# Kernel optimization log

Measured on AMD Instinct MI355X. Metric: run time of the kernel, lower is better.

## Reference

```python
import jax, jax.numpy as jnp
import numpy as np

N_NODES = 35
N_EDGES = 1190
N_VIEWS = 6
C1_IN, C1_OUT = 1, 256
C2_IN, C2_OUT = 256, 256
C3_IN, C3_OUT = 256, 64


def _nnconv(x, edge_attr, src, dst, nn_w, nn_b, lin_w, bias, c_in, c_out):
    """PyG NNConv with aggr='mean': per-edge MLP weight, gather-matvec-scatter."""
    # per-edge weight matrices: [E, c_in, c_out]
    W = jax.nn.relu(edge_attr @ nn_w.T + nn_b).reshape(-1, c_in, c_out)
    # gather source features and apply per-edge weight: [E, c_out]
    msg = jnp.einsum('ei,eio->eo', x[src], W)
    # scatter-mean into target nodes
    agg = jax.ops.segment_sum(msg, dst, num_segments=N_NODES)
    cnt = jax.ops.segment_sum(jnp.ones((msg.shape[0],), msg.dtype), dst,
                              num_segments=N_NODES)
    agg = agg / jnp.maximum(cnt, 1.0)[:, None]
    # root transform (lin has no bias in PyG) + conv bias
    return agg + x @ lin_w.T + bias


def setup_inputs() -> dict:
    key = jax.random.key(0)
    ks = jax.random.split(key, 16)
    s = 0.05
    x = jnp.ones((N_NODES, C1_IN), jnp.float32)
    edge_attr = jax.random.uniform(ks[0], (N_EDGES, N_VIEWS), jnp.float32)
    edge_index = jax.random.randint(ks[1], (2, N_EDGES), 0, N_NODES, jnp.int32)
    inp = {
        'x': x, 'edge_attr': edge_attr, 'edge_index': edge_index,
        'nn1_w': jax.random.normal(ks[2], (C1_IN * C1_OUT, N_VIEWS), jnp.float32) * s,
        'nn1_b': jax.random.normal(ks[3], (C1_IN * C1_OUT,), jnp.float32) * s,
        'lin1_w': jax.random.normal(ks[4], (C1_OUT, C1_IN), jnp.float32) * s,
        'b1': jax.random.normal(ks[5], (C1_OUT,), jnp.float32) * s,
        'nn2_w': jax.random.normal(ks[6], (C2_IN * C2_OUT, N_VIEWS), jnp.float32) * s,
        'nn2_b': jax.random.normal(ks[7], (C2_IN * C2_OUT,), jnp.float32) * s,
        'lin2_w': jax.random.normal(ks[8], (C2_OUT, C2_IN), jnp.float32) * s,
        'b2': jax.random.normal(ks[9], (C2_OUT,), jnp.float32) * s,
        'nn3_w': jax.random.normal(ks[10], (C3_IN * C3_OUT, N_VIEWS), jnp.float32) * s,
        'nn3_b': jax.random.normal(ks[11], (C3_IN * C3_OUT,), jnp.float32) * s,
        'lin3_w': jax.random.normal(ks[12], (C3_OUT, C3_IN), jnp.float32) * s,
        'b3': jax.random.normal(ks[13], (C3_OUT,), jnp.float32) * s,
    }
    return inp


def reference(x, edge_attr, edge_index, nn1_w, nn1_b, lin1_w, b1,
              nn2_w, nn2_b, lin2_w, b2, nn3_w, nn3_b, lin3_w, b3):
    src, dst = edge_index[0], edge_index[1]
    x = jax.nn.relu(_nnconv(x, edge_attr, src, dst, nn1_w, nn1_b, lin1_w, b1, C1_IN, C1_OUT))
    x = jax.nn.relu(_nnconv(x, edge_attr, src, dst, nn2_w, nn2_b, lin2_w, b2, C2_IN, C2_OUT))
    x = jax.nn.relu(_nnconv(x, edge_attr, src, dst, nn3_w, nn3_b, lin3_w, b3, C3_IN, C3_OUT))
    # CBT: pairwise L1 distances over feature dim -> [N, N]
    # (equivalent to repeat(35,1,1) / transpose / abs / sum since N == 35)
    cbt = jnp.abs(x[None, :, :] - x[:, None, :]).sum(-1)
    return cbt
```

## Files before the change

### kernel.cpp

```cpp
#include <hip/hip_runtime.h>


#define NN 35
#define NE 1190
#define TE 10
#define NG 119

__global__ void zero_k(float* p, int n) {
    int t = blockIdx.x * 256 + threadIdx.x;
    if (t < n) p[t] = 0.f;
}

__global__ __launch_bounds__(512) void msg1_k(
    const float* __restrict__ x, const float* __restrict__ ea,
    const int* __restrict__ ei, const float* __restrict__ w1,
    const float* __restrict__ b1w, float* __restrict__ agg1,
    float* __restrict__ cnt) {
    int tid = threadIdx.x;
    int e = blockIdx.x * 2 + (tid >> 8);
    int o = tid & 255;
    int src = ei[e];
    int dst = ei[NE + e];
    float xs = x[src];
    const float* eap = ea + e * 6;
    const float* w = w1 + o * 6;
    float d = b1w[o];
#pragma unroll
    for (int v = 0; v < 6; v++) d = fmaf(eap[v], w[v], d);
    atomicAdd(agg1 + dst * 256 + o, xs * fmaxf(d, 0.f));
    if (o == 0) atomicAdd(cnt + dst, 1.0f);
}

__global__ __launch_bounds__(256) void x1_k(
    const float* __restrict__ x, const float* __restrict__ lin1,
    const float* __restrict__ b1, const float* __restrict__ agg1,
    const float* __restrict__ cnt, float* __restrict__ x1) {
    int n = blockIdx.x, o = threadIdx.x;
    float c = fmaxf(cnt[n], 1.f);
    float v = agg1[n * 256 + o] / c + x[n] * lin1[o] + b1[o];
    x1[n * 256 + o] = fmaxf(v, 0.f);
}

__global__ __launch_bounds__(512, 4) void msg2_k(
    const float* __restrict__ x1, const float* __restrict__ ea,
    const int* __restrict__ ei, const float* __restrict__ w2,
    const float* __restrict__ b2w, float* __restrict__ agg2) {
    __shared__ __attribute__((aligned(16))) float xs[TE][256];
    __shared__ float eas[TE][6];
    __shared__ int dsts[TE];
    __shared__ int srcs[TE];
    __shared__ float part[7][TE][64];
    int tid = threadIdx.x;
    int eg = blockIdx.x >> 2;
    int og = blockIdx.x & 3;
    int e0 = eg * TE;
    if (tid < TE) { dsts[tid] = ei[NE + e0 + tid]; srcs[tid] = ei[e0 + tid]; }
    if (tid >= 64 && tid < 64 + TE * 6) {
        int t = tid - 64;
        eas[t / 6][t % 6] = ea[e0 * 6 + t];
    }
    __syncthreads();
    for (int idx = tid; idx < TE * 64; idx += 512) {
        int te = idx >> 6, q = idx & 63;
        ((float4*)xs[te])[q] = ((const float4*)(x1 + srcs[te] * 256))[q];
    }
    __syncthreads();
    int ol = tid & 63;
    int o = og * 64 + ol;
    int ic = tid >> 6;
    float eareg[TE][6];
#pragma unroll
    for (int te = 0; te < TE; te++)
#pragma unroll
        for (int v = 0; v < 6; v++) eareg[te][v] = eas[te][v];
    float acc[TE] = {};
    for (int ii = 0; ii < 32; ii++) {
        int i = ic * 32 + ii;
        const float* w = w2 + (size_t)(i * 256 + o) * 6;
        float2 wa = *(const float2*)w;
        float2 wb = *(const float2*)(w + 2);
        float2 wc = *(const float2*)(w + 4);
        float b = b2w[i * 256 + o];
#pragma unroll
        for (int te = 0; te < TE; te += 2) {
            float dx = b, dy = b;
            dx = fmaf(eareg[te][0], wa.x, dx); dy = fmaf(eareg[te + 1][0], wa.x, dy);
            dx = fmaf(eareg[te][1], wa.y, dx); dy = fmaf(eareg[te + 1][1], wa.y, dy);
            dx = fmaf(eareg[te][2], wb.x, dx); dy = fmaf(eareg[te + 1][2], wb.x, dy);
            dx = fmaf(eareg[te][3], wb.y, dx); dy = fmaf(eareg[te + 1][3], wb.y, dy);
            dx = fmaf(eareg[te][4], wc.x, dx); dy = fmaf(eareg[te + 1][4], wc.x, dy);
            dx = fmaf(eareg[te][5], wc.y, dx); dy = fmaf(eareg[te + 1][5], wc.y, dy);
            dx = fmaxf(dx, 0.f);               dy = fmaxf(dy, 0.f);
            acc[te] = fmaf(xs[te][i], dx, acc[te]);
            acc[te + 1] = fmaf(xs[te + 1][i], dy, acc[te + 1]);
        }
    }
    if (ic > 0) {
#pragma unroll
        for (int te = 0; te < TE; te++) part[ic - 1][te][ol] = acc[te];
    }
    __syncthreads();
    if (ic == 0) {
#pragma unroll
        for (int te = 0; te < TE; te++) {
            float s = acc[te];
#pragma unroll
            for (int p = 0; p < 7; p++) s += part[p][te][ol];
            atomicAdd(agg2 + dsts[te] * 256 + o, s);
        }
    }
}

__global__ __launch_bounds__(1024) void x2_k(
    const float* __restrict__ x1, const float* __restrict__ lin2,
    const float* __restrict__ b2, const float* __restrict__ agg2,
    const float* __restrict__ cnt, float* __restrict__ x2) {
    __shared__ float xr[256];
    __shared__ float part[3][256];
    int n = blockIdx.x, tid = threadIdx.x;
    int o = tid & 255, ic = tid >> 8;
    if (tid < 256) xr[tid] = x1[n * 256 + tid];
    __syncthreads();
    const float4* w = (const float4*)(lin2 + (size_t)o * 256 + ic * 64);
    float s = 0.f;
#pragma unroll
    for (int k = 0; k < 16; k++) {
        float4 wv = w[k];
        int i = ic * 64 + k * 4;
        s = fmaf(wv.x, xr[i], s);
        s = fmaf(wv.y, xr[i + 1], s);
        s = fmaf(wv.z, xr[i + 2], s);
        s = fmaf(wv.w, xr[i + 3], s);
    }
    if (ic > 0) part[ic - 1][o] = s;
    __syncthreads();
    if (ic == 0) {
        float tot = s + part[0][o] + part[1][o] + part[2][o];
        float c = fmaxf(cnt[n], 1.f);
        float v = agg2[n * 256 + o] / c + tot + b2[o];
        x2[n * 256 + o] = fmaxf(v, 0.f);
    }
}

__global__ __launch_bounds__(512, 4) void msg3_k(
    const float* __restrict__ x2, const float* __restrict__ ea,
    const int* __restrict__ ei, const float* __restrict__ w3,
    const float* __restrict__ b3w, float* __restrict__ agg3) {
    __shared__ __attribute__((aligned(16))) float xs[TE][64];
    __shared__ float eas[TE][6];
    __shared__ int dsts[TE];
    __shared__ int srcs[TE];
    __shared__ float part[7][TE][64];
    int tid = threadIdx.x;
    int eg = blockIdx.x >> 2;
    int ig = blockIdx.x & 3;
    int e0 = eg * TE;
    if (tid < TE) { dsts[tid] = ei[NE + e0 + tid]; srcs[tid] = ei[e0 + tid]; }
    if (tid >= 64 && tid < 64 + TE * 6) {
        int t = tid - 64;
        eas[t / 6][t % 6] = ea[e0 * 6 + t];
    }
    __syncthreads();
    for (int idx = tid; idx < TE * 16; idx += 512) {
        int te = idx >> 4, q = idx & 15;
        ((float4*)xs[te])[q] =
            ((const float4*)(x2 + srcs[te] * 256 + ig * 64))[q];
    }
    __syncthreads();
    int ol = tid & 63;
    int ic = tid >> 6;
    float eareg[TE][6];
#pragma unroll
    for (int te = 0; te < TE; te++)
#pragma unroll
        for (int v = 0; v < 6; v++) eareg[te][v] = eas[te][v];
    float acc[TE] = {};
    for (int jj = 0; jj < 8; jj++) {
        int ii = ic * 8 + jj;
        int i = ig * 64 + ii;
        const float* w = w3 + (size_t)(i * 64 + ol) * 6;
        float2 wa = *(const float2*)w;
        float2 wb = *(const float2*)(w + 2);
        float2 wc = *(const float2*)(w + 4);
        float b = b3w[i * 64 + ol];
#pragma unroll
        for (int te = 0; te < TE; te += 2) {
            float dx = b, dy = b;
            dx = fmaf(eareg[te][0], wa.x, dx); dy = fmaf(eareg[te + 1][0], wa.x, dy);
            dx = fmaf(eareg[te][1], wa.y, dx); dy = fmaf(eareg[te + 1][1], wa.y, dy);
            dx = fmaf(eareg[te][2], wb.x, dx); dy = fmaf(eareg[te + 1][2], wb.x, dy);
            dx = fmaf(eareg[te][3], wb.y, dx); dy = fmaf(eareg[te + 1][3], wb.y, dy);
            dx = fmaf(eareg[te][4], wc.x, dx); dy = fmaf(eareg[te + 1][4], wc.x, dy);
            dx = fmaf(eareg[te][5], wc.y, dx); dy = fmaf(eareg[te + 1][5], wc.y, dy);
            dx = fmaxf(dx, 0.f);               dy = fmaxf(dy, 0.f);
            acc[te] = fmaf(xs[te][ii], dx, acc[te]);
            acc[te + 1] = fmaf(xs[te + 1][ii], dy, acc[te + 1]);
        }
    }
    if (ic > 0) {
#pragma unroll
        for (int te = 0; te < TE; te++) part[ic - 1][te][ol] = acc[te];
    }
    __syncthreads();
    if (ic == 0) {
#pragma unroll
        for (int te = 0; te < TE; te++) {
            float s = acc[te];
#pragma unroll
            for (int p = 0; p < 7; p++) s += part[p][te][ol];
            atomicAdd(agg3 + dsts[te] * 64 + ol, s);
        }
    }
}

__global__ __launch_bounds__(256) void x3_k(
    const float* __restrict__ x2, const float* __restrict__ lin3,
    const float* __restrict__ b3, const float* __restrict__ agg3,
    const float* __restrict__ cnt, float* __restrict__ x3) {
    __shared__ float xr[256];
    __shared__ float part[3][64];
    int n = blockIdx.x, tid = threadIdx.x;
    int o = tid & 63, ic = tid >> 6;
    xr[tid] = x2[n * 256 + tid];
    __syncthreads();
    const float4* w = (const float4*)(lin3 + (size_t)o * 256 + ic * 64);
    float s = 0.f;
#pragma unroll
    for (int k = 0; k < 16; k++) {
        float4 wv = w[k];
        int i = ic * 64 + k * 4;
        s = fmaf(wv.x, xr[i], s);
        s = fmaf(wv.y, xr[i + 1], s);
        s = fmaf(wv.z, xr[i + 2], s);
        s = fmaf(wv.w, xr[i + 3], s);
    }
    if (ic > 0) part[ic - 1][o] = s;
    __syncthreads();
    if (ic == 0) {
        float tot = s + part[0][o] + part[1][o] + part[2][o];
        float c = fmaxf(cnt[n], 1.f);
        x3[n * 64 + o] = fmaxf(agg3[n * 64 + o] / c + tot + b3[o], 0.f);
    }
}

__global__ __launch_bounds__(256) void cbt_k(const float* __restrict__ x3,
                                             float* __restrict__ out) {
    int t = blockIdx.x * 256 + threadIdx.x;
    if (t >= NN * NN) return;
    int i = t / NN, j = t % NN;
    const float* a = x3 + i * 64;
    const float* b = x3 + j * 64;
    float s = 0.f;
#pragma unroll
    for (int f = 0; f < 64; f++) s += fabsf(a[f] - b[f]);
    out[t] = s;
}

extern "C" void kernel_launch(void* const* d_in, const int* in_sizes, int n_in,
                              void* d_out, int out_size, void* d_ws, size_t ws_size,
                              hipStream_t stream) {
    const float* x    = (const float*)d_in[0];
    const float* ea   = (const float*)d_in[1];
    const int*   ei   = (const int*)d_in[2];
    const float* nn1w = (const float*)d_in[3];
    const float* nn1b = (const float*)d_in[4];
    const float* lin1 = (const float*)d_in[5];
    const float* b1   = (const float*)d_in[6];
    const float* nn2w = (const float*)d_in[7];
    const float* nn2b = (const float*)d_in[8];
    const float* lin2 = (const float*)d_in[9];
    const float* b2   = (const float*)d_in[10];
    const float* nn3w = (const float*)d_in[11];
    const float* nn3b = (const float*)d_in[12];
    const float* lin3 = (const float*)d_in[13];
    const float* b3   = (const float*)d_in[14];

    float* ws   = (float*)d_ws;
    float* x1   = ws;
    float* x2   = ws + 8960;
    float* x3v  = ws + 17920;
    float* agg1 = ws + 20160;
    float* agg2 = ws + 29120;
    float* agg3 = ws + 38080;
    float* cnt  = ws + 40320;
    float* out  = (float*)d_out;

    zero_k<<<(20195 + 255) / 256, 256, 0, stream>>>(agg1, 20195);
    msg1_k<<<NE / 2, 512, 0, stream>>>(x, ea, ei, nn1w, nn1b, agg1, cnt);
    x1_k<<<NN, 256, 0, stream>>>(x, lin1, b1, agg1, cnt, x1);
    msg2_k<<<NG * 4, 512, 0, stream>>>(x1, ea, ei, nn2w, nn2b, agg2);
    x2_k<<<NN, 1024, 0, stream>>>(x1, lin2, b2, agg2, cnt, x2);
    msg3_k<<<NG * 4, 512, 0, stream>>>(x2, ea, ei, nn3w, nn3b, agg3);
    x3_k<<<NN, 256, 0, stream>>>(x2, lin3, b3, agg3, cnt, x3v);
    cbt_k<<<(NN * NN + 255) / 256, 256, 0, stream>>>(x3v, out);
}
```

Before: 146.5 us.

## Fuse node-update kernels into following message kernels with recomputation

Removes the separate x1 and x2 node-update kernels. Each message block now recomputes the needed source-node features from agg1/agg2 directly, and extra blocks in the layer-3 kernel write x2 for the final root transform. The zeroing kernel also transposes lin2 for coalesced access. This cuts two launches and their global round trips, at the cost of redundant per-block recomputation of x1 and the lin2 matvec.

```diff
diff --git a/kernel.cpp b/kernel.cpp
--- a/kernel.cpp
+++ b/kernel.cpp
@@ -6,9 +6,25 @@
 #define TE 10
 #define NG 119
 
-__global__ void zero_k(float* p, int n) {
-    int t = blockIdx.x * 256 + threadIdx.x;
-    if (t < n) p[t] = 0.f;
+#define OFF_AGG1 0
+#define OFF_AGG2 8960
+#define OFF_AGG3 17920
+#define OFF_CNT  20160
+#define ZERO_N   20195
+#define OFF_L2T  20224
+#define OFF_X2M  85760
+#define OFF_X3   94720
+
+__global__ __launch_bounds__(256) void prep_k(float* __restrict__ ws,
+                                              const float* __restrict__ lin2) {
+    int b = blockIdx.x, t = threadIdx.x;
+    if (b < 80) {
+        int idx = b * 256 + t;
+        if (idx < ZERO_N) ws[idx] = 0.f;
+    } else {
+        int i = b - 80;
+        ws[OFF_L2T + i * 256 + t] = lin2[t * 256 + i];
+    }
 }
 
 __global__ __launch_bounds__(512) void msg1_k(
@@ -31,38 +47,31 @@
     if (o == 0) atomicAdd(cnt + dst, 1.0f);
 }
 
-__global__ __launch_bounds__(256) void x1_k(
-    const float* __restrict__ x, const float* __restrict__ lin1,
+__global__ __launch_bounds__(512, 4) void msg2x1_k(
+    const float* __restrict__ x, const float* __restrict__ ea,
+    const int* __restrict__ ei, const float* __restrict__ lin1,
     const float* __restrict__ b1, const float* __restrict__ agg1,
-    const float* __restrict__ cnt, float* __restrict__ x1) {
-    int n = blockIdx.x, o = threadIdx.x;
-    float c = fmaxf(cnt[n], 1.f);
-    float v = agg1[n * 256 + o] / c + x[n] * lin1[o] + b1[o];
-    x1[n * 256 + o] = fmaxf(v, 0.f);
-}
-
-__global__ __launch_bounds__(512, 4) void msg2_k(
-    const float* __restrict__ x1, const float* __restrict__ ea,
-    const int* __restrict__ ei, const float* __restrict__ w2,
+    const float* __restrict__ cnt, const float* __restrict__ w2,
     const float* __restrict__ b2w, float* __restrict__ agg2) {
-    __shared__ __attribute__((aligned(16))) float xs[TE][256];
+    __shared__ float xs[TE][256];
     __shared__ float eas[TE][6];
-    __shared__ int dsts[TE];
-    __shared__ int srcs[TE];
+    __shared__ int srcs[TE], dsts[TE];
     __shared__ float part[7][TE][64];
     int tid = threadIdx.x;
-    int eg = blockIdx.x >> 2;
-    int og = blockIdx.x & 3;
+    int eg = blockIdx.x >> 2, og = blockIdx.x & 3;
     int e0 = eg * TE;
-    if (tid < TE) { dsts[tid] = ei[NE + e0 + tid]; srcs[tid] = ei[e0 + tid]; }
+    if (tid < TE) { srcs[tid] = ei[e0 + tid]; dsts[tid] = ei[NE + e0 + tid]; }
     if (tid >= 64 && tid < 64 + TE * 6) {
         int t = tid - 64;
         eas[t / 6][t % 6] = ea[e0 * 6 + t];
     }
     __syncthreads();
-    for (int idx = tid; idx < TE * 64; idx += 512) {
-        int te = idx >> 6, q = idx & 63;
-        ((float4*)xs[te])[q] = ((const float4*)(x1 + srcs[te] * 256))[q];
+    for (int idx = tid; idx < TE * 256; idx += 512) {
+        int te = idx >> 8, i = idx & 255;
+        int s = srcs[te];
+        float c = fmaxf(cnt[s], 1.f);
+        float v = agg1[s * 256 + i] / c + x[s] * lin1[i] + b1[i];
+        xs[te][i] = fmaxf(v, 0.f);
     }
     __syncthreads();
     int ol = tid & 63;
@@ -111,64 +120,92 @@
     }
 }
 
-__global__ __launch_bounds__(1024) void x2_k(
-    const float* __restrict__ x1, const float* __restrict__ lin2,
+__global__ __launch_bounds__(512, 4) void msg3x2_k(
+    const float* __restrict__ x, const float* __restrict__ ea,
+    const int* __restrict__ ei, const float* __restrict__ lin1,
+    const float* __restrict__ b1, const float* __restrict__ agg1,
+    const float* __restrict__ cnt, const float* __restrict__ lin2T,
     const float* __restrict__ b2, const float* __restrict__ agg2,
-    const float* __restrict__ cnt, float* __restrict__ x2) {
-    __shared__ float xr[256];
-    __shared__ float part[3][256];
-    int n = blockIdx.x, tid = threadIdx.x;
-    int o = tid & 255, ic = tid >> 8;
-    if (tid < 256) xr[tid] = x1[n * 256 + tid];
-    __syncthreads();
-    const float4* w = (const float4*)(lin2 + (size_t)o * 256 + ic * 64);
-    float s = 0.f;
-#pragma unroll
-    for (int k = 0; k < 16; k++) {
-        float4 wv = w[k];
-        int i = ic * 64 + k * 4;
-        s = fmaf(wv.x, xr[i], s);
-        s = fmaf(wv.y, xr[i + 1], s);
-        s = fmaf(wv.z, xr[i + 2], s);
-        s = fmaf(wv.w, xr[i + 3], s);
-    }
-    if (ic > 0) part[ic - 1][o] = s;
-    __syncthreads();
-    if (ic == 0) {
-        float tot = s + part[0][o] + part[1][o] + part[2][o];
-        float c = fmaxf(cnt[n], 1.f);
-        float v = agg2[n * 256 + o] / c + tot + b2[o];
-        x2[n * 256 + o] = fmaxf(v, 0.f);
-    }
-}
-
-__global__ __launch_bounds__(512, 4) void msg3_k(
-    const float* __restrict__ x2, const float* __restrict__ ea,
-    const int* __restrict__ ei, const float* __restrict__ w3,
-    const float* __restrict__ b3w, float* __restrict__ agg3) {
-    __shared__ __attribute__((aligned(16))) float xs[TE][64];
+    const float* __restrict__ w3, const float* __restrict__ b3w,
+    float* __restrict__ agg3, float* __restrict__ x2m) {
+    __shared__ float x1r[TE][256];
+    __shared__ float xs[TE][64];
     __shared__ float eas[TE][6];
-    __shared__ int dsts[TE];
-    __shared__ int srcs[TE];
+    __shared__ int srcs[TE], dsts[TE];
     __shared__ float part[7][TE][64];
     int tid = threadIdx.x;
-    int eg = blockIdx.x >> 2;
-    int ig = blockIdx.x & 3;
+
+    if (blockIdx.x >= 476) {
+        int n = blockIdx.x - 476;
+        float c = fmaxf(cnt[n], 1.f);
+        if (tid < 256) {
+            float v = agg1[n * 256 + tid] / c + x[n] * lin1[tid] + b1[tid];
+            x1r[0][tid] = fmaxf(v, 0.f);
+        }
+        __syncthreads();
+        int o = tid & 255, ic = tid >> 8;
+        float s = 0.f;
+        for (int ii = 0; ii < 128; ii++) {
+            int i = ic * 128 + ii;
+            s = fmaf(lin2T[i * 256 + o], x1r[0][i], s);
+        }
+        float* p2 = &part[0][0][0];
+        if (ic == 1) p2[o] = s;
+        __syncthreads();
+        if (ic == 0) {
+            float v = agg2[n * 256 + o] / c + s + p2[o] + b2[o];
+            x2m[n * 256 + o] = fmaxf(v, 0.f);
+        }
+        return;
+    }
+
+    int eg = blockIdx.x >> 2, ig = blockIdx.x & 3;
     int e0 = eg * TE;
-    if (tid < TE) { dsts[tid] = ei[NE + e0 + tid]; srcs[tid] = ei[e0 + tid]; }
+    if (tid < TE) { srcs[tid] = ei[e0 + tid]; dsts[tid] = ei[NE + e0 + tid]; }
     if (tid >= 64 && tid < 64 + TE * 6) {
         int t = tid - 64;
         eas[t / 6][t % 6] = ea[e0 * 6 + t];
     }
     __syncthreads();
-    for (int idx = tid; idx < TE * 16; idx += 512) {
-        int te = idx >> 4, q = idx & 15;
-        ((float4*)xs[te])[q] =
-            ((const float4*)(x2 + srcs[te] * 256 + ig * 64))[q];
+    for (int idx = tid; idx < TE * 256; idx += 512) {
+        int te = idx >> 8, i = idx & 255;
+        int s = srcs[te];
+        float c = fmaxf(cnt[s], 1.f);
+        float v = agg1[s * 256 + i] / c + x[s] * lin1[i] + b1[i];
+        x1r[te][i] = fmaxf(v, 0.f);
     }
     __syncthreads();
     int ol = tid & 63;
     int ic = tid >> 6;
+    int o2 = ig * 64 + ol;
+    {
+        float acc2[TE] = {};
+        for (int ii = 0; ii < 32; ii++) {
+            int i = ic * 32 + ii;
+            float w = lin2T[i * 256 + o2];
+#pragma unroll
+            for (int te = 0; te < TE; te++)
+                acc2[te] = fmaf(w, x1r[te][i], acc2[te]);
+        }
+        if (ic > 0) {
+#pragma unroll
+            for (int te = 0; te < TE; te++) part[ic - 1][te][ol] = acc2[te];
+        }
+        __syncthreads();
+        if (ic == 0) {
+#pragma unroll
+            for (int te = 0; te < TE; te++) {
+                float ssum = acc2[te];
+#pragma unroll
+                for (int p = 0; p < 7; p++) ssum += part[p][te][ol];
+                int s = srcs[te];
+                float c = fmaxf(cnt[s], 1.f);
+                float v = agg2[s * 256 + o2] / c + ssum + b2[o2];
+                xs[te][ol] = fmaxf(v, 0.f);
+            }
+        }
+        __syncthreads();
+    }
     float eareg[TE][6];
 #pragma unroll
     for (int te = 0; te < TE; te++)
@@ -214,14 +251,14 @@
 }
 
 __global__ __launch_bounds__(256) void x3_k(
-    const float* __restrict__ x2, const float* __restrict__ lin3,
+    const float* __restrict__ x2m, const float* __restrict__ lin3,
     const float* __restrict__ b3, const float* __restrict__ agg3,
     const float* __restrict__ cnt, float* __restrict__ x3) {
     __shared__ float xr[256];
     __shared__ float part[3][64];
     int n = blockIdx.x, tid = threadIdx.x;
     int o = tid & 63, ic = tid >> 6;
-    xr[tid] = x2[n * 256 + tid];
+    xr[tid] = x2m[n * 256 + tid];
     __syncthreads();
     const float4* w = (const float4*)(lin3 + (size_t)o * 256 + ic * 64);
     float s = 0.f;
@@ -275,22 +312,23 @@
     const float* lin3 = (const float*)d_in[13];
     const float* b3   = (const float*)d_in[14];
 
-    float* ws   = (float*)d_ws;
-    float* x1   = ws;
-    float* x2   = ws + 8960;
-    float* x3v  = ws + 17920;
-    float* agg1 = ws + 20160;
-    float* agg2 = ws + 29120;
-    float* agg3 = ws + 38080;
-    float* cnt  = ws + 40320;
-    float* out  = (float*)d_out;
-
-    zero_k<<<(20195 + 255) / 256, 256, 0, stream>>>(agg1, 20195);
+    float* ws    = (float*)d_ws;
+    float* agg1  = ws + OFF_AGG1;
+    float* agg2  = ws + OFF_AGG2;
+    float* agg3  = ws + OFF_AGG3;
+    float* cnt   = ws + OFF_CNT;
+    float* lin2T = ws + OFF_L2T;
+    float* x2m   = ws + OFF_X2M;
+    float* x3v   = ws + OFF_X3;
+    float* out   = (float*)d_out;
+
+    prep_k<<<336, 256, 0, stream>>>(ws, lin2);
     msg1_k<<<NE / 2, 512, 0, stream>>>(x, ea, ei, nn1w, nn1b, agg1, cnt);
-    x1_k<<<NN, 256, 0, stream>>>(x, lin1, b1, agg1, cnt, x1);
-    msg2_k<<<NG * 4, 512, 0, stream>>>(x1, ea, ei, nn2w, nn2b, agg2);
-    x2_k<<<NN, 1024, 0, stream>>>(x1, lin2, b2, agg2, cnt, x2);
-    msg3_k<<<NG * 4, 512, 0, stream>>>(x2, ea, ei, nn3w, nn3b, agg3);
-    x3_k<<<NN, 256, 0, stream>>>(x2, lin3, b3, agg3, cnt, x3v);
+    msg2x1_k<<<NG * 4, 512, 0, stream>>>(x, ea, ei, lin1, b1, agg1, cnt,
+                                         nn2w, nn2b, agg2);
+    msg3x2_k<<<NG * 4 + NN, 512, 0, stream>>>(x, ea, ei, lin1, b1, agg1, cnt,
+                                              lin2T, b2, agg2, nn3w, nn3b,
+                                              agg3, x2m);
+    x3_k<<<NN, 256, 0, stream>>>(x2m, lin3, b3, agg3, cnt, x3v);
     cbt_k<<<(NN * NN + 255) / 256, 256, 0, stream>>>(x3v, out);
 }
```

Result: faster. 140.0 us (-4.4%).
